# Performance work log

Hardware: AMD Instinct MI355X
Metric: run time of the kernel (lower is better)

Reference implementation:

```python
import jax, jax.numpy as jnp
import numpy as np

H = 8  # n_heads (init_kwarg, closed over)


def setup_inputs() -> dict:
    key = jax.random.key(0)
    ks = jax.random.split(key, 5)
    B, T, D, L = 8, 4096, 512, 128
    # lecun_normal: std = 1/sqrt(fan_in), fan_in = first dim here
    X = jax.random.normal(ks[0], (B, T, D), dtype=jnp.float32)
    Wk = jax.random.normal(ks[1], (D, L), dtype=jnp.float32) / np.sqrt(D)
    Wq = jax.random.normal(ks[2], (D, L), dtype=jnp.float32) / np.sqrt(D)
    Wv = jax.random.normal(ks[3], (D, D), dtype=jnp.float32) / np.sqrt(D)
    o_proj = jax.random.normal(ks[4], (D, D), dtype=jnp.float32) / np.sqrt(D)
    return {"X": X, "Wk": Wk, "Wq": Wq, "Wv": Wv, "o_proj": o_proj}


def reference(X, Wk, Wq, Wv, o_proj):
    B, T, D = X.shape
    L = Wk.shape[1]
    Dh, Lh = D // H, L // H
    # time-major projections: (T, B, H, *)
    V = jnp.einsum('DM,BTD->TBM', Wv, X).reshape(T, B, H, Dh)
    Q = jnp.einsum('DL,BTD->TBL', Wq, X).reshape(T, B, H, Lh)
    K = jnp.einsum('DL,BTD->TBL', Wk, X).reshape(T, B, H, Lh)
    scale = jax.lax.rsqrt(jnp.array(Dh, dtype=jnp.float32))
    K_exp = jnp.exp(K * scale)                      # (T,B,H,Lh)
    alpha = jnp.cumsum(K_exp, axis=0)               # causal normalizer
    Qs = jax.nn.softmax(Q * scale, axis=-1) / alpha # (T,B,H,Lh)

    def step(carry, args):
        qs_t, ke_t, v_t = args
        carry = carry + jnp.einsum('bhl,bhd->bhld', ke_t, v_t)
        y_t = jnp.einsum('bhl,bhld->bhd', qs_t, carry)
        return carry, y_t

    init = jnp.zeros((B, H, Lh, Dh), dtype=X.dtype)
    _, y = jax.lax.scan(step, init, (Qs, K_exp, V), unroll=16)  # y: (T,B,H,Dh)
    # faithful to source: transpose(3,0,1,2) then reshape(B,T,D)
    y = y.transpose(3, 0, 1, 2).reshape(B, T, D)
    return y @ o_proj
```

## Files before the change

kernel.cpp:

```cpp
#include <hip/hip_runtime.h>
#include <hip/hip_bf16.h>

#define B_ 8
#define T_ 4096
#define D_ 512
#define L_ 128
#define H_ 8
#define Dh_ 64
#define Lh_ 16
#define M_ (B_*T_)
#define SCALE 0.125f

typedef __bf16 v8bf __attribute__((ext_vector_type(8)));
typedef float  v4f  __attribute__((ext_vector_type(4)));
typedef unsigned short u16;
typedef u16 v8u __attribute__((ext_vector_type(8)));

__device__ __forceinline__ float b2f(u16 h){
    unsigned int u = ((unsigned int)h) << 16;
    return __builtin_bit_cast(float, u);
}
__device__ __forceinline__ u16 f2bf(float f){
    unsigned int u = __builtin_bit_cast(unsigned int, f);
    u += 0x7FFFu + ((u >> 16) & 1u);
    return (u16)(u >> 16);
}

__device__ __forceinline__ void gload16(const u16* g, u16* l) {
    __builtin_amdgcn_global_load_lds(
        (const __attribute__((address_space(1))) unsigned int*)(g),
        (__attribute__((address_space(3))) unsigned int*)(l), 16, 0, 0);
}

__global__ __launch_bounds__(256) void prep(
        const float* __restrict__ X,  const float* __restrict__ Wq,
        const float* __restrict__ Wk, const float* __restrict__ Wv,
        const float* __restrict__ Wo,
        u16* __restrict__ Xb, u16* __restrict__ WT, u16* __restrict__ OT)
{
    int bid = blockIdx.x;
    if (bid < 8192) {
        const size_t i = (size_t)bid * 256 + threadIdx.x;
        const float4* s = (const float4*)X + i * 2;
        float4 a = s[0], b = s[1];
        v8u o;
        o[0] = f2bf(a.x); o[1] = f2bf(a.y); o[2] = f2bf(a.z); o[3] = f2bf(a.w);
        o[4] = f2bf(b.x); o[5] = f2bf(b.y); o[6] = f2bf(b.z); o[7] = f2bf(b.w);
        *((v8u*)Xb + i) = o;
        return;
    }
    bid -= 8192;
    const float* src; u16* dst; int cols, bx, by;
    if (bid < 64)       { src = Wq; dst = WT;             cols = 128; bx = bid & 3;  by = bid >> 2; }
    else if (bid < 128) { src = Wk; dst = WT + 128 * 512; cols = 128; bid -= 64;  bx = bid & 3;  by = bid >> 2; }
    else if (bid < 384) { src = Wv; dst = WT + 256 * 512; cols = 512; bid -= 128; bx = bid & 15; by = bid >> 4; }
    else                { src = Wo; dst = OT;             cols = 512; bid -= 384; bx = bid & 15; by = bid >> 4; }
    __shared__ u16 tile[32][33];
    const int tx = threadIdx.x & 31, ty = threadIdx.x >> 5;
    const int c0 = bx * 32, r0 = by * 32;
    #pragma unroll
    for (int i = 0; i < 32; i += 8)
        tile[ty + i][tx] = f2bf(src[(size_t)(r0 + ty + i) * cols + c0 + tx]);
    __syncthreads();
    #pragma unroll
    for (int i = 0; i < 32; i += 8)
        dst[(size_t)(c0 + ty + i) * 512 + r0 + tx] = tile[tx][ty + i];
}

template<int MODE, int NY>
__global__ __launch_bounds__(256) void gemm_mfma(
        const u16* __restrict__ A, const u16* __restrict__ Bt,
        float* __restrict__ Qo, u16* __restrict__ KEo,
        u16* __restrict__ Vo, float* __restrict__ OutF)
{
    __shared__ __align__(16) u16 As[128 * 64];
    __shared__ __align__(16) u16 Bs[128 * 64];
    const int tid  = threadIdx.x;
    const int wave = tid >> 6, lane = tid & 63;
    const int wm = wave >> 1, wn = wave & 1;
    const int lm = lane & 15, quad = lane >> 4;

    const int bid = blockIdx.x;
    const int xcd = bid & 7, idx = bid >> 3;
    const int bx  = xcd * 32 + idx / NY;
    const int by  = idx % NY;
    const int gm0 = bx * 128, gn0 = by * 128;

    const int srow0 = wave * 32 + (lane >> 3);
    const int sg    = lane & 7;

    v4f acc[4][4];
    #pragma unroll
    for (int i = 0; i < 4; i++)
        #pragma unroll
        for (int j = 0; j < 4; j++)
            acc[i][j] = (v4f){0.f, 0.f, 0.f, 0.f};

    for (int kt = 0; kt < 8; ++kt) {
        const int k0 = kt * 64;
        #pragma unroll
        for (int r = 0; r < 4; ++r) {
            const int row = srow0 + r * 8;
            const int col = ((sg ^ (row & 7)) << 3) + k0;
            gload16(&A [(size_t)(gm0 + row) * 512 + col], &As[(wave * 4 + r) * 512]);
            gload16(&Bt[(size_t)(gn0 + row) * 512 + col], &Bs[(wave * 4 + r) * 512]);
        }
        __syncthreads();
        v8bf af[2][4], bfr[2][4];
        #pragma unroll
        for (int ks = 0; ks < 2; ks++)
            #pragma unroll
            for (int mi = 0; mi < 4; mi++) {
                const int g  = ks * 4 + quad;
                const int ra = wm * 64 + mi * 16 + lm;
                const int rb = wn * 64 + mi * 16 + lm;
                af [ks][mi] = *(const v8bf*)&As[ra * 64 + ((g ^ (ra & 7)) << 3)];
                bfr[ks][mi] = *(const v8bf*)&Bs[rb * 64 + ((g ^ (rb & 7)) << 3)];
            }
        #pragma unroll
        for (int ks = 0; ks < 2; ks++)
            #pragma unroll
            for (int mi = 0; mi < 4; mi++)
                #pragma unroll
                for (int ni = 0; ni < 4; ni++)
                    acc[mi][ni] = __builtin_amdgcn_mfma_f32_16x16x32_bf16(
                                      af[ks][mi], bfr[ks][ni], acc[mi][ni], 0, 0, 0);
        __syncthreads();
    }

    if (MODE == 1) {
        #pragma unroll
        for (int mi = 0; mi < 4; mi++)
          #pragma unroll
          for (int ni = 0; ni < 4; ni++)
            #pragma unroll
            for (int i = 0; i < 4; i++) {
                int row = gm0 + wm * 64 + mi * 16 + quad * 4 + i;
                int col = gn0 + wn * 64 + ni * 16 + lm;
                OutF[(size_t)row * 512 + col] = acc[mi][ni][i];
            }
    } else if (gn0 == 0) {
        #pragma unroll
        for (int mi = 0; mi < 4; mi++)
          #pragma unroll
          for (int ni = 0; ni < 4; ni++)
            #pragma unroll
            for (int i = 0; i < 4; i++) {
                int row = gm0 + wm * 64 + mi * 16 + quad * 4 + i;
                int col = wn * 64 + ni * 16 + lm;
                float qv = acc[mi][ni][i] * SCALE;
                float m = qv;
                #pragma unroll
                for (int off = 1; off < 16; off <<= 1) m = fmaxf(m, __shfl_xor(m, off));
                float e = __expf(qv - m);
                float s = e;
                #pragma unroll
                for (int off = 1; off < 16; off <<= 1) s += __shfl_xor(s, off);
                Qo[(size_t)row * 128 + col] = e / s;
            }
    } else if (gn0 == 128) {
        #pragma unroll
        for (int mi = 0; mi < 4; mi++)
          #pragma unroll
          for (int ni = 0; ni < 4; ni++)
            #pragma unroll
            for (int i = 0; i < 4; i++) {
                int row = gm0 + wm * 64 + mi * 16 + quad * 4 + i;
                int col = wn * 64 + ni * 16 + lm;
                KEo[(size_t)row * 128 + col] = f2bf(__expf(acc[mi][ni][i] * SCALE));
            }
    } else {
        #pragma unroll
        for (int mi = 0; mi < 4; mi++)
          #pragma unroll
          for (int ni = 0; ni < 4; ni++)
            #pragma unroll
            for (int i = 0; i < 4; i++) {
                int row = gm0 + wm * 64 + mi * 16 + quad * 4 + i;
                int col = gn0 + wn * 64 + ni * 16 + lm - 256;
                Vo[(size_t)row * 512 + col] = f2bf(acc[mi][ni][i]);
            }
    }
}

__global__ __launch_bounds__(256, 2) void chunk_sums_mfma(
        const u16* __restrict__ KE, const u16* __restrict__ V,
        float* __restrict__ Mc, float* __restrict__ AB)
{
    struct CLDS { u16 KA[16][72]; u16 VT[64][72]; };
    __shared__ __align__(16) CLDS lds[4];
    const int tid = threadIdx.x, wave = tid >> 6, lane = tid & 63;
    const int lm = lane & 15, quad = lane >> 4;
    const int ch = blockIdx.x * 4 + wave;
    const int bh = ch >> 6, c = ch & 63, b = bh >> 3, h = bh & 7;
    const int t0 = b * T_ + c * 64;
    CLDS& L = lds[wave];

    {
        const u16* kp = KE + (size_t)(t0 + lane) * L_ + h * Lh_;
        v8u k0 = *(const v8u*)kp, k1 = *(const v8u*)(kp + 8);
        #pragma unroll
        for (int l = 0; l < 8; l++) L.KA[l][lane]     = k0[l];
        #pragma unroll
        for (int l = 0; l < 8; l++) L.KA[l + 8][lane] = k1[l];
        const u16* vp = V + (size_t)(t0 + lane) * D_ + h * Dh_;
        #pragma unroll
        for (int seg = 0; seg < 8; ++seg) {
            v8u pv = *(const v8u*)(vp + seg * 8);
            #pragma unroll
            for (int j = 0; j < 8; j++) L.VT[seg * 8 + j][lane] = pv[j];
        }
    }
    __syncthreads();

    v8bf ka[2];
    #pragma unroll
    for (int ki = 0; ki < 2; ki++)
        ka[ki] = *(const v8bf*)&L.KA[lm][ki * 32 + quad * 8];

    v8u onesu;
    #pragma unroll
    for (int j = 0; j < 8; j++) onesu[j] = 0x3F80;
    v8bf ones = __builtin_bit_cast(v8bf, onesu);

    v4f accL = (v4f){0.f, 0.f, 0.f, 0.f};
    accL = __builtin_amdgcn_mfma_f32_16x16x32_bf16(ka[0], ones, accL, 0, 0, 0);
    accL = __builtin_amdgcn_mfma_f32_16x16x32_bf16(ka[1], ones, accL, 0, 0, 0);

    v4f accM[4];
    #pragma unroll
    for (int nd = 0; nd < 4; nd++) accM[nd] = (v4f){0.f, 0.f, 0.f, 0.f};
    #pragma unroll
    for (int nd = 0; nd < 4; nd++)
        #pragma unroll
        for (int ki = 0; ki < 2; ki++) {
            v8bf vb = *(const v8bf*)&L.VT[nd * 16 + lm][ki * 32 + quad * 8];
            accM[nd] = __builtin_amdgcn_mfma_f32_16x16x32_bf16(ka[ki], vb, accM[nd], 0, 0, 0);
        }

    float* mcb = Mc + (size_t)ch * 1024;
    #pragma unroll
    for (int nd = 0; nd < 4; nd++)
        #pragma unroll
        for (int i = 0; i < 4; i++)
            mcb[(quad * 4 + i) * 64 + nd * 16 + lm] = accM[nd][i];
    if (lm == 0) {
        #pragma unroll
        for (int i = 0; i < 4; i++) AB[ch * 16 + quad * 4 + i] = accL[i];
    }
}

__global__ __launch_bounds__(256) void chunk_prefix(
        const float* __restrict__ Mc, u16* __restrict__ McB,
        float* __restrict__ AB)
{
    const int bh = blockIdx.x >> 2, qq = blockIdx.x & 3;
    const int i = qq * 256 + threadIdx.x;
    const size_t base = (size_t)bh * 64 * 1024 + i;
    float v[64];
    #pragma unroll
    for (int c = 0; c < 64; ++c) v[c] = Mc[base + (size_t)c * 1024];
    float run = 0.f;
    #pragma unroll
    for (int c = 0; c < 64; ++c) {
        McB[base + (size_t)c * 1024] = f2bf(run);
        run += v[c];
    }
    if (qq == 0 && threadIdx.x < 16) {
        const int l = threadIdx.x;
        float a[64];
        #pragma unroll
        for (int c = 0; c < 64; ++c) a[c] = AB[(bh * 64 + c) * 16 + l];
        float r2 = 0.f;
        #pragma unroll
        for (int c = 0; c < 64; ++c) {
            AB[(bh * 64 + c) * 16 + l] = r2;
            r2 += a[c];
        }
    }
}

__global__ __launch_bounds__(256, 2) void intra_mfma(
        const float* __restrict__ QS, const u16* __restrict__ KE,
        const u16* __restrict__ V, const u16* __restrict__ McB,
        const float* __restrict__ AB, u16* __restrict__ Y)
{
    struct ILDS {
        union {
            struct { u16 KA[16][72]; u16 Sc[16][72]; u16 qs[64][40]; } s;
            u16 p[64][72];
        } r;
        u16 VT[64][72];
    };
    __shared__ __align__(16) ILDS lds[4];
    const int tid = threadIdx.x, wave = tid >> 6, lane = tid & 63;
    const int lm = lane & 15, quad = lane >> 4;
    const int ch = blockIdx.x * 4 + wave;
    const int bh = ch >> 6, c = ch & 63, b = bh >> 3, h = bh & 7;
    const int t0 = b * T_ + c * 64;
    ILDS& L = lds[wave];

    {
        const u16* kp = KE + (size_t)(t0 + lane) * L_ + h * Lh_;
        v8u k0 = *(const v8u*)kp, k1 = *(const v8u*)(kp + 8);
        #pragma unroll
        for (int l = 0; l < 8; l++) L.r.s.KA[l][lane]     = k0[l];
        #pragma unroll
        for (int l = 0; l < 8; l++) L.r.s.KA[l + 8][lane] = k1[l];
        const u16* vp = V + (size_t)(t0 + lane) * D_ + h * Dh_;
        #pragma unroll
        for (int seg = 0; seg < 8; ++seg) {
            v8u pv = *(const v8u*)(vp + seg * 8);
            #pragma unroll
            for (int j = 0; j < 8; j++) L.VT[seg * 8 + j][lane] = pv[j];
        }
        const u16* mcb = McB + (size_t)ch * 1024;
        #pragma unroll
        for (int l = 0; l < 16; l++)
            L.r.s.Sc[l][lane] = mcb[l * 64 + lane];
        v8u z8;
        #pragma unroll
        for (int j = 0; j < 8; j++) z8[j] = 0;
        *(v8u*)&L.r.s.qs[lane][16] = z8;
        *(v8u*)&L.r.s.qs[lane][24] = z8;
    }
    const float ab = AB[ch * 16 + lm];
    __syncthreads();

    v4f acc_a[4];
    #pragma unroll
    for (int mi = 0; mi < 4; mi++) acc_a[mi] = (v4f){ab, ab, ab, ab};
    #pragma unroll
    for (int mi = 0; mi < 4; mi++)
        #pragma unroll
        for (int ki = 0; ki < 2; ki++) {
            if (ki == 1 && mi < 2) continue;
            v8u ta;
            #pragma unroll
            for (int j = 0; j < 8; j++)
                ta[j] = (ki * 32 + quad * 8 + j <= mi * 16 + lm) ? (u16)0x3F80 : (u16)0;
            v8bf kb = *(const v8bf*)&L.r.s.KA[lm][ki * 32 + quad * 8];
            acc_a[mi] = __builtin_amdgcn_mfma_f32_16x16x32_bf16(
                            __builtin_bit_cast(v8bf, ta), kb, acc_a[mi], 0, 0, 0);
        }

    #pragma unroll
    for (int mi = 0; mi < 4; mi++)
        #pragma unroll
        for (int i = 0; i < 4; i++) {
            int t = mi * 16 + quad * 4 + i;
            float qs = QS[(size_t)(t0 + t) * L_ + h * Lh_ + lm];
            L.r.s.qs[t][lm] = f2bf(qs / acc_a[mi][i]);
        }
    __syncthreads();

    v8bf aq[4];
    #pragma unroll
    for (int mi = 0; mi < 4; mi++)
        aq[mi] = *(const v8bf*)&L.r.s.qs[mi * 16 + lm][quad * 8];

    v4f accP[4][4], accY[4][4];
    #pragma unroll
    for (int mi = 0; mi < 4; mi++)
        #pragma unroll
        for (int ni = 0; ni < 4; ni++) {
            accP[mi][ni] = (v4f){0.f, 0.f, 0.f, 0.f};
            accY[mi][ni] = (v4f){0.f, 0.f, 0.f, 0.f};
        }

    #pragma unroll
    for (int ni = 0; ni < 4; ni++) {
        v8u kbu;
        #pragma unroll
        for (int j = 0; j < 8; j++) kbu[j] = 0;
        if (quad < 2) {
            #pragma unroll
            for (int j = 0; j < 8; j++)
                kbu[j] = L.r.s.KA[quad * 8 + j][ni * 16 + lm];
        }
        v8bf kbf = __builtin_bit_cast(v8bf, kbu);
        #pragma unroll
        for (int mi = ni; mi < 4; mi++)
            accP[mi][ni] = __builtin_amdgcn_mfma_f32_16x16x32_bf16(
                               aq[mi], kbf, accP[mi][ni], 0, 0, 0);
    }
    #pragma unroll
    for (int nd = 0; nd < 4; nd++) {
        v8u scu;
        #pragma unroll
        for (int j = 0; j < 8; j++) scu[j] = 0;
        if (quad < 2) {
            #pragma unroll
            for (int j = 0; j < 8; j++)
                scu[j] = L.r.s.Sc[quad * 8 + j][nd * 16 + lm];
        }
        v8bf scf = __builtin_bit_cast(v8bf, scu);
        #pragma unroll
        for (int mi = 0; mi < 4; mi++)
            accY[mi][nd] = __builtin_amdgcn_mfma_f32_16x16x32_bf16(
                               aq[mi], scf, accY[mi][nd], 0, 0, 0);
    }
    __syncthreads();

    #pragma unroll
    for (int mi = 0; mi < 4; mi++)
        #pragma unroll
        for (int ni = 0; ni < 4; ni++)
            #pragma unroll
            for (int i = 0; i < 4; i++) {
                int t = mi * 16 + quad * 4 + i, tp = ni * 16 + lm;
                float pv = (ni < mi) ? accP[mi][ni][i]
                          : (ni == mi ? ((tp <= t) ? accP[mi][ni][i] : 0.f) : 0.f);
                L.r.p[t][tp] = f2bf(pv);
            }
    __syncthreads();

    v8bf vb[4][2];
    #pragma unroll
    for (int nd = 0; nd < 4; nd++)
        #pragma unroll
        for (int ki = 0; ki < 2; ki++)
            vb[nd][ki] = *(const v8bf*)&L.VT[nd * 16 + lm][ki * 32 + quad * 8];
    #pragma unroll
    for (int mi = 0; mi < 4; mi++)
        #pragma unroll
        for (int ki = 0; ki < 2; ki++) {
            if (ki == 1 && mi < 2) continue;
            v8bf pa = *(const v8bf*)&L.r.p[mi * 16 + lm][ki * 32 + quad * 8];
            #pragma unroll
            for (int nd = 0; nd < 4; nd++)
                accY[mi][nd] = __builtin_amdgcn_mfma_f32_16x16x32_bf16(
                                   pa, vb[nd][ki], accY[mi][nd], 0, 0, 0);
        }

    #pragma unroll
    for (int mi = 0; mi < 4; mi++)
        #pragma unroll
        for (int nd = 0; nd < 4; nd++)
            #pragma unroll
            for (int i = 0; i < 4; i++) {
                int t = mi * 16 + quad * 4 + i;
                Y[(((size_t)(c * 64 + t)) * 64 + bh) * 64 + nd * 16 + lm] =
                    f2bf(accY[mi][nd][i]);
            }
}

__global__ __launch_bounds__(64) void transpose_Y(
        const u16* __restrict__ Y, u16* __restrict__ Z)
{
    __shared__ __align__(16) u16 tile[64][72];
    const int g = blockIdx.x, t = threadIdx.x;
    const u16* yp = Y + (size_t)(g * 64 + t) * 64;
    #pragma unroll
    for (int seg = 0; seg < 8; ++seg)
        *(v8u*)&tile[t][seg * 8] = *(const v8u*)(yp + seg * 8);
    __syncthreads();
    const int cl = t & 7, dq = t >> 3;
    #pragma unroll
    for (int p = 0; p < 8; ++p) {
        const int dh = p * 8 + dq;
        v8u pk;
        #pragma unroll
        for (int j = 0; j < 8; j++) pk[j] = tile[cl * 8 + j][dh];
        *(v8u*)&Z[(size_t)dh * 262144 + (size_t)g * 64 + cl * 8] = pk;
    }
}

extern "C" void kernel_launch(void* const* d_in, const int* in_sizes, int n_in,
                              void* d_out, int out_size, void* d_ws, size_t ws_size,
                              hipStream_t stream)
{
    (void)in_sizes; (void)n_in; (void)out_size; (void)ws_size;
    const float* X  = (const float*)d_in[0];
    const float* Wk = (const float*)d_in[1];
    const float* Wq = (const float*)d_in[2];
    const float* Wv = (const float*)d_in[3];
    const float* Wo = (const float*)d_in[4];
    float* Out = (float*)d_out;

    char* p = (char*)d_ws;
    auto alloc = [&](size_t bytes) { char* r = p; p += (bytes + 255) & ~(size_t)255; return r; };
    u16*   Xb = (u16*)  alloc((size_t)M_ * 512 * 2);
    u16*   WT = (u16*)  alloc((size_t)768 * 512 * 2);
    u16*   OT = (u16*)  alloc((size_t)512 * 512 * 2);
    u16*   V  = (u16*)  alloc((size_t)M_ * 512 * 2);
    float* Mc = (float*)alloc((size_t)4096 * 1024 * 4);
    float* AB = (float*)alloc((size_t)4096 * 16 * 4);
    float* Q  = (float*)alloc((size_t)M_ * 128 * 4);
    u16*   KE = (u16*)  alloc((size_t)M_ * 128 * 2);
    u16*   Y  = (u16*)  alloc((size_t)M_ * 512 * 2);
    u16*   Z  = (u16*)Mc;
    u16*   McB = (u16*)Xb;

    prep<<<8832, 256, 0, stream>>>(X, Wq, Wk, Wv, Wo, Xb, WT, OT);

    gemm_mfma<0, 6><<<1536, 256, 0, stream>>>(Xb, WT, Q, KE, V, nullptr);
    chunk_sums_mfma<<<1024, 256, 0, stream>>>(KE, V, Mc, AB);
    chunk_prefix   <<<256,  256, 0, stream>>>(Mc, McB, AB);
    intra_mfma     <<<1024, 256, 0, stream>>>(Q, KE, V, McB, AB, Y);
    transpose_Y    <<<4096, 64,  0, stream>>>(Y, Z);
    gemm_mfma<1, 4><<<1024, 256, 0, stream>>>(Z, OT, nullptr, nullptr, nullptr, Out);
}
```

Before: 254.6 us.

## Use wave-local fences, regroup GEMM tile order, batch transpose into 4-wave blocks

Replaces block-wide __syncthreads with compiler-only fences in chunk kernels where each wave owns its own LDS region, removing barrier stalls. Remaps GEMM block indices so groups of 8 M-tiles share N-tiles within an XCD for better L2 reuse. Packs four independent 64-thread transpose tiles into one 256-thread block with wave-local fences. The compiler fence does not emit a hardware wait on LDS traffic, so correctness relies on single-wave ownership and in-order LDS behaviour within a wave.

```diff
diff --git a/kernel.cpp b/kernel.cpp
--- a/kernel.cpp
+++ b/kernel.cpp
@@ -24,6 +24,10 @@
     unsigned int u = __builtin_bit_cast(unsigned int, f);
     u += 0x7FFFu + ((u >> 16) & 1u);
     return (u16)(u >> 16);
+}
+
+__device__ __forceinline__ void wave_fence() {
+    asm volatile("" ::: "memory");
 }
 
 __device__ __forceinline__ void gload16(const u16* g, u16* l) {
@@ -81,9 +85,10 @@
     const int lm = lane & 15, quad = lane >> 4;
 
     const int bid = blockIdx.x;
-    const int xcd = bid & 7, idx = bid >> 3;
-    const int bx  = xcd * 32 + idx / NY;
-    const int by  = idx % NY;
+    const int xcd = bid & 7, j = bid >> 3;
+    const int grp = j / (8 * NY), r = j % (8 * NY);
+    const int by  = r >> 3, pin = r & 7;
+    const int bx  = xcd * 32 + grp * 8 + pin;
     const int gm0 = bx * 128, gn0 = by * 128;
 
     const int srow0 = wave * 32 + (lane >> 3);
@@ -93,17 +98,17 @@
     #pragma unroll
     for (int i = 0; i < 4; i++)
         #pragma unroll
-        for (int j = 0; j < 4; j++)
-            acc[i][j] = (v4f){0.f, 0.f, 0.f, 0.f};
+        for (int j2 = 0; j2 < 4; j2++)
+            acc[i][j2] = (v4f){0.f, 0.f, 0.f, 0.f};
 
     for (int kt = 0; kt < 8; ++kt) {
         const int k0 = kt * 64;
         #pragma unroll
-        for (int r = 0; r < 4; ++r) {
-            const int row = srow0 + r * 8;
+        for (int rr = 0; rr < 4; ++rr) {
+            const int row = srow0 + rr * 8;
             const int col = ((sg ^ (row & 7)) << 3) + k0;
-            gload16(&A [(size_t)(gm0 + row) * 512 + col], &As[(wave * 4 + r) * 512]);
-            gload16(&Bt[(size_t)(gn0 + row) * 512 + col], &Bs[(wave * 4 + r) * 512]);
+            gload16(&A [(size_t)(gm0 + row) * 512 + col], &As[(wave * 4 + rr) * 512]);
+            gload16(&Bt[(size_t)(gn0 + row) * 512 + col], &Bs[(wave * 4 + rr) * 512]);
         }
         __syncthreads();
         v8bf af[2][4], bfr[2][4];
@@ -211,7 +216,7 @@
             for (int j = 0; j < 8; j++) L.VT[seg * 8 + j][lane] = pv[j];
         }
     }
-    __syncthreads();
+    wave_fence();
 
     v8bf ka[2];
     #pragma unroll
@@ -325,7 +330,7 @@
         *(v8u*)&L.r.s.qs[lane][24] = z8;
     }
     const float ab = AB[ch * 16 + lm];
-    __syncthreads();
+    wave_fence();
 
     v4f acc_a[4];
     #pragma unroll
@@ -352,7 +357,7 @@
             float qs = QS[(size_t)(t0 + t) * L_ + h * Lh_ + lm];
             L.r.s.qs[t][lm] = f2bf(qs / acc_a[mi][i]);
         }
-    __syncthreads();
+    wave_fence();
 
     v8bf aq[4];
     #pragma unroll
@@ -400,7 +405,7 @@
             accY[mi][nd] = __builtin_amdgcn_mfma_f32_16x16x32_bf16(
                                aq[mi], scf, accY[mi][nd], 0, 0, 0);
     }
-    __syncthreads();
+    wave_fence();
 
     #pragma unroll
     for (int mi = 0; mi < 4; mi++)
@@ -413,7 +418,7 @@
                           : (ni == mi ? ((tp <= t) ? accP[mi][ni][i] : 0.f) : 0.f);
                 L.r.p[t][tp] = f2bf(pv);
             }
-    __syncthreads();
+    wave_fence();
 
     v8bf vb[4][2];
     #pragma unroll
@@ -445,23 +450,25 @@
             }
 }
 
-__global__ __launch_bounds__(64) void transpose_Y(
+__global__ __launch_bounds__(256) void transpose_Y(
         const u16* __restrict__ Y, u16* __restrict__ Z)
 {
-    __shared__ __align__(16) u16 tile[64][72];
-    const int g = blockIdx.x, t = threadIdx.x;
+    __shared__ __align__(16) u16 tile[4][64][72];
+    const int wave = threadIdx.x >> 6, t = threadIdx.x & 63;
+    const int g = blockIdx.x * 4 + wave;
+    u16 (*tl)[72] = tile[wave];
     const u16* yp = Y + (size_t)(g * 64 + t) * 64;
     #pragma unroll
     for (int seg = 0; seg < 8; ++seg)
-        *(v8u*)&tile[t][seg * 8] = *(const v8u*)(yp + seg * 8);
-    __syncthreads();
+        *(v8u*)&tl[t][seg * 8] = *(const v8u*)(yp + seg * 8);
+    wave_fence();
     const int cl = t & 7, dq = t >> 3;
     #pragma unroll
     for (int p = 0; p < 8; ++p) {
         const int dh = p * 8 + dq;
         v8u pk;
         #pragma unroll
-        for (int j = 0; j < 8; j++) pk[j] = tile[cl * 8 + j][dh];
+        for (int j = 0; j < 8; j++) pk[j] = tl[cl * 8 + j][dh];
         *(v8u*)&Z[(size_t)dh * 262144 + (size_t)g * 64 + cl * 8] = pk;
     }
 }
@@ -498,6 +505,6 @@
     chunk_sums_mfma<<<1024, 256, 0, stream>>>(KE, V, Mc, AB);
     chunk_prefix   <<<256,  256, 0, stream>>>(Mc, McB, AB);
     intra_mfma     <<<1024, 256, 0, stream>>>(Q, KE, V, McB, AB, Y);
-    transpose_Y    <<<4096, 64,  0, stream>>>(Y, Z);
+    transpose_Y    <<<1024, 256, 0, stream>>>(Y, Z);
     gemm_mfma<1, 4><<<1024, 256, 0, stream>>>(Z, OT, nullptr, nullptr, nullptr, Out);
 }
```

After: 248.5 us. 1.02x faster.
